# Performance work log

Hardware: AMD Instinct MI355X
Metric: run time of the kernel (lower is better)

The kernel has to match this reference:

```python
import jax, jax.numpy as jnp
import numpy as np

B, L, D = 4, 16384, 128          # batch, voxels per sample, d_model
DI, DS, DTR, K = 256, 16, 8, 4   # d_inner, d_state, dt_rank, conv kernel
N = B * L
EPS = 1e-5


def setup_inputs() -> dict:
    key = jax.random.key(0)
    ks = jax.random.split(key, 12)
    s = 0.02
    feats = jax.random.normal(ks[0], (N, D), jnp.float32)
    coords_xyz = jax.random.randint(ks[1], (N, 3), 0, 1024, jnp.int32)
    # per-batch Morton permutation + its inverse
    perm = jnp.stack([jax.random.permutation(jax.random.fold_in(ks[2], i), L) for i in range(B)]).astype(jnp.int32)
    inv_perm = jnp.argsort(perm, axis=1).astype(jnp.int32)
    return {
        'feats': feats,
        'pos_w': jax.random.normal(ks[3], (3, D), jnp.float32) * s,
        'pos_b': jnp.zeros((D,), jnp.float32),
        'rms_w': jnp.ones((D,), jnp.float32),
        'in_proj_w': jax.random.normal(ks[4], (D, 2 * DI), jnp.float32) * s,
        'conv_w': jax.random.normal(ks[5], (DI, K), jnp.float32) * s,
        'conv_b': jnp.zeros((DI,), jnp.float32),
        'x_proj_w': jax.random.normal(ks[6], (DI, DTR + 2 * DS), jnp.float32) * s,
        'dt_proj_w': jax.random.normal(ks[7], (DTR, DI), jnp.float32) * s,
        'dt_proj_b': jax.random.normal(ks[8], (DI,), jnp.float32) * 0.1,
        'A_log': jnp.log(jnp.broadcast_to(jnp.arange(1.0, DS + 1.0, dtype=jnp.float32), (DI, DS))),
        'D_param': jnp.ones((DI,), jnp.float32),
        'out_proj_w': jax.random.normal(ks[9], (DI, D), jnp.float32) * s,
        'ln_w': jnp.ones((D,), jnp.float32),
        'ln_b': jnp.zeros((D,), jnp.float32),
        'coords_xyz': coords_xyz,
        'perm': perm,
        'inv_perm': inv_perm,
    }


def _gssm(feats, pos_w, pos_b, rms_w, in_proj_w, conv_w, conv_b, x_proj_w,
          dt_proj_w, dt_proj_b, A_log, D_param, out_proj_w, ln_w, ln_b,
          coords_xyz, perm, inv_perm):
    # positional embedding of voxel coords
    pe = coords_xyz.astype(jnp.float32) @ pos_w + pos_b            # [N, D]
    h = (feats + pe).reshape(B, L, D)
    # gather into Morton order (per-batch fancy index)
    hm = jnp.take_along_axis(h, perm[:, :, None].astype(jnp.int32), axis=1)  # [B, L, D]
    # Mamba block: RMSNorm then mixer (block returns mixer output only)
    x = hm * jax.lax.rsqrt(jnp.mean(hm * hm, axis=-1, keepdims=True) + EPS) * rms_w
    xz = x @ in_proj_w                                             # [B, L, 2*DI]
    xi, z = xz[..., :DI], xz[..., DI:]
    # depthwise causal conv1d, kernel K
    xp = jnp.pad(xi, ((0, 0), (K - 1, 0), (0, 0)))
    xc = conv_b + sum(xp[:, j:j + L, :] * conv_w[:, j] for j in range(K))
    xc = jax.nn.silu(xc)                                           # [B, L, DI]
    dbc = xc @ x_proj_w                                            # [B, L, DTR+2*DS]
    dt, Bm, Cm = dbc[..., :DTR], dbc[..., DTR:DTR + DS], dbc[..., DTR + DS:]
    dt = jax.nn.softplus(dt @ dt_proj_w + dt_proj_b)               # [B, L, DI]
    A = -jnp.exp(A_log)                                            # [DI, DS]

    def step(hst, inp):
        x_t, dt_t, b_t, c_t = inp                                  # [B,DI],[B,DI],[B,DS],[B,DS]
        hst = jnp.exp(dt_t[..., None] * A) * hst + (dt_t * x_t)[..., None] * b_t[:, None, :]
        return hst, jnp.einsum('bds,bs->bd', hst, c_t)

    h0 = jnp.zeros((B, DI, DS), xc.dtype)
    _, ys = jax.lax.scan(step, h0, (xc.transpose(1, 0, 2), dt.transpose(1, 0, 2),
                                    Bm.transpose(1, 0, 2), Cm.transpose(1, 0, 2)))
    y = ys.transpose(1, 0, 2) + xc * D_param                       # [B, L, DI]
    y = y * jax.nn.silu(z)
    out = y @ out_proj_w                                           # [B, L, D]
    # scatter back to original voxel order
    out = jnp.take_along_axis(out, inv_perm[:, :, None].astype(jnp.int32), axis=1).reshape(N, D)
    # post-SSM LayerNorm
    mu = jnp.mean(out, axis=-1, keepdims=True)
    var = jnp.mean((out - mu) ** 2, axis=-1, keepdims=True)
    return (out - mu) * jax.lax.rsqrt(var + EPS) * ln_w + ln_b


def reference(feats, pos_w, pos_b, rms_w, in_proj_w, conv_w, conv_b, x_proj_w,
              dt_proj_w, dt_proj_b, A_log, D_param, out_proj_w, ln_w, ln_b,
              coords_xyz, perm, inv_perm):
    return _gssm(feats, pos_w, pos_b, rms_w, in_proj_w, conv_w, conv_b, x_proj_w,
                 dt_proj_w, dt_proj_b, A_log, D_param, out_proj_w, ln_w, ln_b,
                 coords_xyz, perm, inv_perm)
```

## Files before the change

### kernel.cpp

```cpp
#include <hip/hip_runtime.h>
#include <hip/hip_bf16.h>
#include <math.h>

#define B_   4
#define L_   16384
#define D_   128
#define DI_  256
#define DS_  16
#define DTR_ 8
#define N_   65536
#define NC_  128
#define LC_  128
#define TW_  16
#define TP_  260
#define EPS_ 1e-5f

typedef __hip_bfloat16 bf16;
typedef __attribute__((ext_vector_type(8))) short short8;
typedef __attribute__((ext_vector_type(4))) float f32x4;

__device__ __forceinline__ bool probe_bf16(const void* Dp) {
  return ((const unsigned*)Dp)[0] == 0x3F803F80u;
}
__device__ __forceinline__ float ldin(const void* p, size_t i, bool isb) {
  return isb ? __bfloat162float(((const bf16*)p)[i]) : ((const float*)p)[i];
}
__device__ __forceinline__ float4 ld4(const void* p, size_t i4, bool isb) {
  if (!isb) return ((const float4*)p)[i4];
  const ushort4 v = ((const ushort4*)p)[i4];
  float4 r;
  r.x = __uint_as_float((unsigned)v.x << 16);
  r.y = __uint_as_float((unsigned)v.y << 16);
  r.z = __uint_as_float((unsigned)v.z << 16);
  r.w = __uint_as_float((unsigned)v.w << 16);
  return r;
}
__device__ __forceinline__ void splitbf(float v, ushort& hi, ushort& lo) {
  bf16 h = __float2bfloat16(v);
  float rem = v - __bfloat162float(h);
  bf16 l = __float2bfloat16(rem);
  hi = *(ushort*)&h;
  lo = *(ushort*)&l;
}


__global__ __launch_bounds__(256) void k_xnorm(
    const void* __restrict__ feats, const void* __restrict__ pos_w,
    const void* __restrict__ pos_b, const void* __restrict__ rms_w,
    const int* __restrict__ coords, const int* __restrict__ perm,
    const void* __restrict__ Dprobe,
    ushort* __restrict__ xh, ushort* __restrict__ xl) {
  const bool isb = probe_bf16(Dprobe);
  int wv = threadIdx.x >> 6, lane = threadIdx.x & 63;
  int p = blockIdx.x * 4 + wv;
  int b = p >> 14;
  int srow = b * L_ + perm[p];
  float cx = (float)coords[srow*3+0];
  float cy = (float)coords[srow*3+1];
  float cz = (float)coords[srow*3+2];
  int i0 = lane, i1 = lane + 64;
  float h0 = ldin(feats,(size_t)srow*D_ + i0,isb) + cx*ldin(pos_w,i0,isb) + cy*ldin(pos_w,D_+i0,isb)
           + cz*ldin(pos_w,2*D_+i0,isb) + ldin(pos_b,i0,isb);
  float h1 = ldin(feats,(size_t)srow*D_ + i1,isb) + cx*ldin(pos_w,i1,isb) + cy*ldin(pos_w,D_+i1,isb)
           + cz*ldin(pos_w,2*D_+i1,isb) + ldin(pos_b,i1,isb);
  float ss = h0*h0 + h1*h1;
  #pragma unroll
  for (int off = 32; off; off >>= 1) ss += __shfl_xor(ss, off);
  float r = 1.0f / sqrtf(ss * (1.f/128.f) + EPS_);
  float v0 = h0 * r * ldin(rms_w,i0,isb);
  float v1 = h1 * r * ldin(rms_w,i1,isb);
  ushort a, bq;
  splitbf(v0, a, bq);
  xh[(size_t)p*D_ + i0] = a; xl[(size_t)p*D_ + i0] = bq;
  splitbf(v1, a, bq);
  xh[(size_t)p*D_ + i1] = a; xl[(size_t)p*D_ + i1] = bq;
}

__global__ __launch_bounds__(256) void k_prepw(
    const void* __restrict__ Win, const void* __restrict__ Dprobe,
    ushort* __restrict__ wth, ushort* __restrict__ wtl) {
  const bool isb = probe_bf16(Dprobe);
  int idx = blockIdx.x * 256 + threadIdx.x;
  int k = idx >> 9, n = idx & 511;
  float v = ldin(Win, (size_t)k*512 + n, isb);
  ushort a, b;
  splitbf(v, a, b);
  wth[(size_t)n*128 + k] = a;
  wtl[(size_t)n*128 + k] = b;
}

__global__ __launch_bounds__(256) void k_prepxw(
    const void* __restrict__ xW, const void* __restrict__ Dprobe,
    ushort* __restrict__ wxh, ushort* __restrict__ wxl) {
  const bool isb = probe_bf16(Dprobe);
  int idx = blockIdx.x * 256 + threadIdx.x;
  int q = idx >> 8, c = idx & 255;
  float v = (q < 40) ? ldin(xW, (size_t)c*40 + q, isb) : 0.f;
  ushort a, b;
  splitbf(v, a, b);
  wxh[idx] = a;
  wxl[idx] = b;
}

__global__ __launch_bounds__(256) void k_prepdtw(
    const void* __restrict__ dtW, const void* __restrict__ Dprobe,
    ushort* __restrict__ dtwh, ushort* __restrict__ dtwl) {
  const bool isb = probe_bf16(Dprobe);
  int idx = blockIdx.x * 256 + threadIdx.x;
  int d = idx >> 5, k = idx & 31;
  float v = (k < 8) ? ldin(dtW, (size_t)k*256 + d, isb) : 0.f;
  ushort a, b;
  splitbf(v, a, b);
  dtwh[idx] = a;
  dtwl[idx] = b;
}

__global__ __launch_bounds__(256) void k_inproj(
    const ushort* __restrict__ xh, const ushort* __restrict__ xl,
    const ushort* __restrict__ wth, const ushort* __restrict__ wtl,
    float* __restrict__ xiT, float* __restrict__ zB) {
  __shared__ short Ah[64*136];
  __shared__ short Al[64*136];
  __shared__ short Bh[32*136];
  __shared__ short Bl[32*136];
  int tid = threadIdx.x;
  int T0 = blockIdx.x * 64;
  int lane = tid & 63, w = tid >> 6;
  {
    int k0 = (tid & 15) * 8;
    int m0 = tid >> 4;
    #pragma unroll
    for (int mi = 0; mi < 4; ++mi) {
      int m = m0 + 16*mi;
      *(short8*)&Ah[m*136 + k0] = *(const short8*)&xh[(size_t)(T0+m)*128 + k0];
      *(short8*)&Al[m*136 + k0] = *(const short8*)&xl[(size_t)(T0+m)*128 + k0];
    }
  }
  __syncthreads();
  int mloc = lane & 15, quad = lane >> 4;
  short8 afh[4], afl[4];
  #pragma unroll
  for (int ks = 0; ks < 4; ++ks) {
    int ka = ks*32 + quad*8;
    afh[ks] = *(const short8*)&Ah[(w*16 + mloc)*136 + ka];
    afl[ks] = *(const short8*)&Al[(w*16 + mloc)*136 + ka];
  }
  for (int ct = 0; ct < 16; ++ct) {
    int C0 = ct * 32;
    __syncthreads();
    {
      int k0 = (tid & 15) * 8;
      int n0 = tid >> 4;
      #pragma unroll
      for (int ni = 0; ni < 2; ++ni) {
        int n = n0 + 16*ni;
        *(short8*)&Bh[n*136 + k0] = *(const short8*)&wth[(size_t)(C0+n)*128 + k0];
        *(short8*)&Bl[n*136 + k0] = *(const short8*)&wtl[(size_t)(C0+n)*128 + k0];
      }
    }
    __syncthreads();
    #pragma unroll
    for (int nt = 0; nt < 2; ++nt) {
      f32x4 acc = {0.f, 0.f, 0.f, 0.f};
      #pragma unroll
      for (int ks = 0; ks < 4; ++ks) {
        int kb = ks*32 + quad*8;
        short8 bh = *(const short8*)&Bh[(nt*16 + mloc)*136 + kb];
        short8 bl = *(const short8*)&Bl[(nt*16 + mloc)*136 + kb];
        acc = __builtin_amdgcn_mfma_f32_16x16x32_bf16(afh[ks], bh, acc, 0, 0, 0);
        acc = __builtin_amdgcn_mfma_f32_16x16x32_bf16(afl[ks], bh, acc, 0, 0, 0);
        acc = __builtin_amdgcn_mfma_f32_16x16x32_bf16(afh[ks], bl, acc, 0, 0, 0);
      }
      int col = C0 + nt*16 + mloc;
      int trow = T0 + w*16 + quad*4;
      if (col < 256) {
        *(float4*)&xiT[(size_t)col*N_ + trow] = make_float4(acc[0], acc[1], acc[2], acc[3]);
      } else {
        int zc = col - 256;
        #pragma unroll
        for (int r = 0; r < 4; ++r)
          zB[(size_t)(trow + r)*256 + zc] = acc[r];
      }
    }
  }
}

__global__ __launch_bounds__(256) void k_conv_s(
    const float* __restrict__ xiT, const void* __restrict__ conv_w,
    const void* __restrict__ conv_b, const void* __restrict__ Dprobe,
    float* __restrict__ xcT) {
  const bool isb = probe_bf16(Dprobe);
  int idx = blockIdx.x * 256 + threadIdx.x;
  int c = idx >> 16;
  int t = idx & 65535;
  int l = t & (L_-1);
  const float* row = xiT + (size_t)c * N_;
  float acc = ldin(conv_b, c, isb);
  if (l >= 3) acc += row[t-3] * ldin(conv_w, c*4+0, isb);
  if (l >= 2) acc += row[t-2] * ldin(conv_w, c*4+1, isb);
  if (l >= 1) acc += row[t-1] * ldin(conv_w, c*4+2, isb);
  acc += row[t] * ldin(conv_w, c*4+3, isb);
  xcT[(size_t)c*N_ + t] = acc / (1.f + __expf(-acc));
}

__global__ __launch_bounds__(256) void k_xproj(
    const float* __restrict__ xcT,
    const ushort* __restrict__ wxh, const ushort* __restrict__ wxl,
    const ushort* __restrict__ dtwh, const ushort* __restrict__ dtwl,
    const void* __restrict__ dtb, const void* __restrict__ Dprobe,
    float* __restrict__ dtT, float* __restrict__ BmB, float* __restrict__ CmB) {
  const bool isb = probe_bf16(Dprobe);
  __shared__ float s40[64*52];
  __shared__ float sdtb[256];
  const int tid = threadIdx.x;
  const int lane = tid & 63, w = tid >> 6;
  const int T0 = blockIdx.x * 64;
  const int n15 = lane & 15, quad = lane >> 4;
  sdtb[tid] = ldin(dtb, tid, isb);

  f32x4 acc0 = {0.f,0.f,0.f,0.f}, acc1 = {0.f,0.f,0.f,0.f}, acc2 = {0.f,0.f,0.f,0.f};
  const float* xb = &xcT[(size_t)(quad*8)*N_ + T0 + w*16 + n15];
  #pragma unroll
  for (int ks = 0; ks < 8; ++ks) {
    short8 bh, bl;
    #pragma unroll
    for (int j = 0; j < 8; ++j) {
      ushort h, l;
      splitbf(xb[(size_t)(ks*32 + j)*N_], h, l);
      bh[j] = (short)h; bl[j] = (short)l;
    }
    #pragma unroll
    for (int mt = 0; mt < 3; ++mt) {
      const size_t aoff = (size_t)(mt*16 + n15)*256 + ks*32 + quad*8;
      short8 ah = *(const short8*)&wxh[aoff];
      short8 al = *(const short8*)&wxl[aoff];
      f32x4 a = (mt==0) ? acc0 : (mt==1) ? acc1 : acc2;
      a = __builtin_amdgcn_mfma_f32_16x16x32_bf16(ah, bh, a, 0, 0, 0);
      a = __builtin_amdgcn_mfma_f32_16x16x32_bf16(al, bh, a, 0, 0, 0);
      a = __builtin_amdgcn_mfma_f32_16x16x32_bf16(ah, bl, a, 0, 0, 0);
      if (mt==0) acc0 = a; else if (mt==1) acc1 = a; else acc2 = a;
    }
  }
  {
    const int trow = (w*16 + n15)*52;
    #pragma unroll
    for (int r = 0; r < 4; ++r) {
      s40[trow +      quad*4 + r] = acc0[r];
      s40[trow + 16 + quad*4 + r] = acc1[r];
      s40[trow + 32 + quad*4 + r] = acc2[r];
    }
  }
  __syncthreads();
  {
    int t = tid >> 2, fq = tid & 3;
    float4 bm = *(const float4*)&s40[t*52 + 8  + fq*4];
    float4 cm = *(const float4*)&s40[t*52 + 24 + fq*4];
    *(float4*)&BmB[(size_t)(T0+t)*16 + fq*4] = bm;
    *(float4*)&CmB[(size_t)(T0+t)*16 + fq*4] = cm;
  }
  short8 dh, dl;
  #pragma unroll
  for (int j = 0; j < 8; ++j) {
    ushort h, l;
    splitbf(s40[(w*16 + n15)*52 + quad*8 + j], h, l);
    dh[j] = (short)h; dl[j] = (short)l;
  }
  #pragma unroll
  for (int mt = 0; mt < 16; ++mt) {
    f32x4 a = {0.f,0.f,0.f,0.f};
    const size_t doff = (size_t)(mt*16 + n15)*32 + quad*8;
    short8 ah = *(const short8*)&dtwh[doff];
    short8 al = *(const short8*)&dtwl[doff];
    a = __builtin_amdgcn_mfma_f32_16x16x32_bf16(ah, dh, a, 0, 0, 0);
    a = __builtin_amdgcn_mfma_f32_16x16x32_bf16(al, dh, a, 0, 0, 0);
    a = __builtin_amdgcn_mfma_f32_16x16x32_bf16(ah, dl, a, 0, 0, 0);
    #pragma unroll
    for (int r = 0; r < 4; ++r) {
      int d = mt*16 + quad*4 + r;
      float pre = a[r] + sdtb[d];
      float sp = (pre > 20.f) ? pre : log1pf(__expf(pre));
      dtT[(size_t)d*N_ + T0 + w*16 + n15] = sp;
    }
  }
}

__global__ __launch_bounds__(256) void k_scan1(
    const float* __restrict__ dtT, const float* __restrict__ xcT,
    const float* __restrict__ BmB, const void* __restrict__ A_log,
    const void* __restrict__ Dprobe, float* __restrict__ Pb, float* __restrict__ Sb) {
  const bool isb = probe_bf16(Dprobe);
  __shared__ float sdt[TW_*TP_];
  __shared__ float sxc[TW_*TP_];
  __shared__ float sbm[LC_*16];
  int tid = threadIdx.x;
  int blk = blockIdx.x;
  int b = blk >> 7, ch = blk & 127;
  int T0 = b * L_ + ch * LC_;
  int d = tid;
  #pragma unroll
  for (int p = 0; p < 2; ++p) {
    int f = (p*256 + tid) * 4;
    *(float4*)&sbm[f] = *(const float4*)&BmB[(size_t)T0*16 + f];
  }
  float Al[16];
  #pragma unroll
  for (int s = 0; s < 16; ++s) Al[s] = -__expf(ldin(A_log, d*16 + s, isb));
  float h[16];
  #pragma unroll
  for (int s = 0; s < 16; ++s) h[s] = 0.f;
  float sumdt = 0.f;
  for (int it = 0; it < LC_; it += TW_) {
    __syncthreads();
    #pragma unroll
    for (int p = 0; p < 4; ++p) {
      int idx = p*256 + tid;
      int d2 = idx >> 2;
      int i4 = (idx & 3) * 4;
      float4 v = *(const float4*)&dtT[(size_t)d2*N_ + T0 + it + i4];
      float4 w = *(const float4*)&xcT[(size_t)d2*N_ + T0 + it + i4];
      sdt[(i4+0)*TP_ + d2] = v.x; sdt[(i4+1)*TP_ + d2] = v.y;
      sdt[(i4+2)*TP_ + d2] = v.z; sdt[(i4+3)*TP_ + d2] = v.w;
      sxc[(i4+0)*TP_ + d2] = w.x; sxc[(i4+1)*TP_ + d2] = w.y;
      sxc[(i4+2)*TP_ + d2] = w.z; sxc[(i4+3)*TP_ + d2] = w.w;
    }
    __syncthreads();
    #pragma unroll
    for (int i = 0; i < TW_; ++i) {
      float dtv = sdt[i*TP_ + d];
      float xcv = sxc[i*TP_ + d];
      sumdt += dtv;
      float du = dtv * xcv;
      const float* bmr = &sbm[(it+i)*16];
      #pragma unroll
      for (int s = 0; s < 16; ++s)
        h[s] = __expf(dtv * Al[s]) * h[s] + du * bmr[s];
    }
  }
  size_t rec = ((size_t)blk*256 + d) * 16;
  #pragma unroll
  for (int s = 0; s < 16; ++s) {
    Sb[rec + s] = h[s];
    Pb[rec + s] = __expf(Al[s] * sumdt);
  }
}

__global__ __launch_bounds__(256) void k_scan2(
    const float* __restrict__ Pb, const float* __restrict__ Sb, float* __restrict__ Hin) {
  int tid = blockIdx.x * 256 + threadIdx.x;
  int b = tid >> 12, r = tid & 4095;
  float h = 0.f;
  for (int ch = 0; ch < NC_; ++ch) {
    size_t rec = ((size_t)(b*NC_ + ch)) * 4096 + r;
    Hin[rec] = h;
    h = Pb[rec] * h + Sb[rec];
  }
}

__global__ __launch_bounds__(256) void k_scan3(
    const float* __restrict__ dtT, const float* __restrict__ xcT,
    const float* __restrict__ BmB, const float* __restrict__ CmB,
    const void* __restrict__ A_log, const void* __restrict__ Dp,
    const float* __restrict__ Hin, float* __restrict__ zyg) {
  const bool isb = probe_bf16(Dp);
  __shared__ float sdt[TW_*TP_];
  __shared__ float sxc[TW_*TP_];
  __shared__ float sbm[LC_*16];
  __shared__ float scm[LC_*16];
  int tid = threadIdx.x;
  int blk = blockIdx.x;
  int b = blk >> 7, ch = blk & 127;
  int T0 = b * L_ + ch * LC_;
  int d = tid;
  #pragma unroll
  for (int p = 0; p < 2; ++p) {
    int f = (p*256 + tid) * 4;
    *(float4*)&sbm[f] = *(const float4*)&BmB[(size_t)T0*16 + f];
    *(float4*)&scm[f] = *(const float4*)&CmB[(size_t)T0*16 + f];
  }
  float Al[16];
  #pragma unroll
  for (int s = 0; s < 16; ++s) Al[s] = -__expf(ldin(A_log, d*16 + s, isb));
  float h[16];
  size_t rec = ((size_t)blk*256 + d) * 16;
  #pragma unroll
  for (int s = 0; s < 16; ++s) h[s] = Hin[rec + s];
  float Dv = ldin(Dp, d, isb);
  for (int it = 0; it < LC_; it += TW_) {
    __syncthreads();
    #pragma unroll
    for (int p = 0; p < 4; ++p) {
      int idx = p*256 + tid;
      int d2 = idx >> 2;
      int i4 = (idx & 3) * 4;
      float4 v = *(const float4*)&dtT[(size_t)d2*N_ + T0 + it + i4];
      float4 w = *(const float4*)&xcT[(size_t)d2*N_ + T0 + it + i4];
      sdt[(i4+0)*TP_ + d2] = v.x; sdt[(i4+1)*TP_ + d2] = v.y;
      sdt[(i4+2)*TP_ + d2] = v.z; sdt[(i4+3)*TP_ + d2] = v.w;
      sxc[(i4+0)*TP_ + d2] = w.x; sxc[(i4+1)*TP_ + d2] = w.y;
      sxc[(i4+2)*TP_ + d2] = w.z; sxc[(i4+3)*TP_ + d2] = w.w;
    }
    __syncthreads();
    #pragma unroll
    for (int i = 0; i < TW_; ++i) {
      float dtv = sdt[i*TP_ + d];
      float xcv = sxc[i*TP_ + d];
      float du = dtv * xcv;
      const float* bmr = &sbm[(it+i)*16];
      const float* cmr = &scm[(it+i)*16];
      float y = 0.f;
      #pragma unroll
      for (int s = 0; s < 16; ++s) {
        h[s] = __expf(dtv * Al[s]) * h[s] + du * bmr[s];
        y += h[s] * cmr[s];
      }
      float yv = y + xcv * Dv;
      size_t zi = (size_t)(T0 + it + i)*256 + d;
      float zv = zyg[zi];
      float sil = zv / (1.f + __expf(-zv));
      zyg[zi] = yv * sil;
    }
  }
}

__global__ __launch_bounds__(256) void k_outproj(
    const float* __restrict__ yg, const void* __restrict__ W2,
    const void* __restrict__ Dprobe, float* __restrict__ outp) {
  const bool isb = probe_bf16(Dprobe);
  __shared__ float As[64*68];
  __shared__ float Bs[64*128];
  int tid = threadIdx.x;
  int T0 = blockIdx.x * 64;
  int tm = tid & 15, tn = tid >> 4;
  float acc[4][8] = {{0.f}};
  for (int kb = 0; kb < 256; kb += 64) {
    {
      int m = tid & 63, kq = tid >> 6;
      #pragma unroll
      for (int r = 0; r < 4; ++r) {
        int k0 = kq*16 + r*4;
        float4 v = *(const float4*)&yg[(size_t)(T0+m)*256 + kb + k0];
        As[(k0+0)*68+m] = v.x; As[(k0+1)*68+m] = v.y;
        As[(k0+2)*68+m] = v.z; As[(k0+3)*68+m] = v.w;
      }
      int n = (tid & 31)*4, kq2 = tid >> 5;
      #pragma unroll
      for (int p = 0; p < 8; ++p) {
        int k = kq2 + p*8;
        float4 w = ld4(W2, ((size_t)(kb+k)*128 + n) >> 2, isb);
        *(float4*)&Bs[k*128 + n] = w;
      }
    }
    __syncthreads();
    #pragma unroll 4
    for (int k = 0; k < 64; ++k) {
      float4 a  = *(const float4*)&As[k*68 + tm*4];
      float4 b0 = *(const float4*)&Bs[k*128 + tn*8];
      float4 b1 = *(const float4*)&Bs[k*128 + tn*8 + 4];
      float am[4] = {a.x, a.y, a.z, a.w};
      float bn[8] = {b0.x, b0.y, b0.z, b0.w, b1.x, b1.y, b1.z, b1.w};
      #pragma unroll
      for (int mi = 0; mi < 4; ++mi)
        #pragma unroll
        for (int ni = 0; ni < 8; ++ni)
          acc[mi][ni] += am[mi] * bn[ni];
    }
    __syncthreads();
  }
  #pragma unroll
  for (int mi = 0; mi < 4; ++mi) {
    size_t m = (size_t)(T0 + tm*4 + mi);
    *(float4*)&outp[m*128 + tn*8]     = make_float4(acc[mi][0], acc[mi][1], acc[mi][2], acc[mi][3]);
    *(float4*)&outp[m*128 + tn*8 + 4] = make_float4(acc[mi][4], acc[mi][5], acc[mi][6], acc[mi][7]);
  }
}

__global__ __launch_bounds__(256) void k_ln(
    const float* __restrict__ outp, const int* __restrict__ perm,
    const void* __restrict__ ln_w, const void* __restrict__ ln_b,
    const void* __restrict__ Dprobe, void* __restrict__ out) {
  const bool isb = probe_bf16(Dprobe);
  int wv = threadIdx.x >> 6, lane = threadIdx.x & 63;
  int p = blockIdx.x * 4 + wv;
  int b = p >> 14;
  int dest = b * L_ + perm[p];
  float v0 = outp[(size_t)p*128 + lane];
  float v1 = outp[(size_t)p*128 + lane + 64];
  float s1 = v0 + v1, s2 = v0*v0 + v1*v1;
  #pragma unroll
  for (int off = 32; off; off >>= 1) {
    s1 += __shfl_xor(s1, off);
    s2 += __shfl_xor(s2, off);
  }
  float mean = s1 * (1.f/128.f);
  float var  = s2 * (1.f/128.f) - mean*mean;
  float r = 1.0f / sqrtf(var + EPS_);
  float o0 = (v0 - mean)*r*ldin(ln_w,lane,isb)    + ldin(ln_b,lane,isb);
  float o1 = (v1 - mean)*r*ldin(ln_w,lane+64,isb) + ldin(ln_b,lane+64,isb);
  if (isb) {
    ((bf16*)out)[(size_t)dest*128 + lane]      = __float2bfloat16(o0);
    ((bf16*)out)[(size_t)dest*128 + lane + 64] = __float2bfloat16(o1);
  } else {
    ((float*)out)[(size_t)dest*128 + lane]      = o0;
    ((float*)out)[(size_t)dest*128 + lane + 64] = o1;
  }
}

extern "C" void kernel_launch(void* const* d_in, const int* in_sizes, int n_in,
                              void* d_out, int out_size, void* d_ws, size_t ws_size,
                              hipStream_t stream) {
  const void* feats    = d_in[0];
  const void* pos_w    = d_in[1];
  const void* pos_b    = d_in[2];
  const void* rms_w    = d_in[3];
  const void* in_proj  = d_in[4];
  const void* conv_w   = d_in[5];
  const void* conv_b   = d_in[6];
  const void* x_proj   = d_in[7];
  const void* dt_projw = d_in[8];
  const void* dt_projb = d_in[9];
  const void* A_log    = d_in[10];
  const void* D_param  = d_in[11];
  const void* out_proj = d_in[12];
  const void* ln_w     = d_in[13];
  const void* ln_b     = d_in[14];
  const int*  coords   = (const int*)d_in[15];
  const int*  perm     = (const int*)d_in[16];

  float* ws = (float*)d_ws;
  const size_t NN = (size_t)N_;
  ushort* xh  = (ushort*)ws;
  ushort* xl  = (ushort*)(ws + 64*NN);
  ushort* wth = (ushort*)(ws + 640*NN);
  ushort* wtl = (ushort*)(ws + 641*NN);
  ushort* wxh  = (ushort*)ws;
  ushort* wxl  = ((ushort*)ws) + 12288;
  ushort* dtwh = ((ushort*)ws) + 24576;
  ushort* dtwl = ((ushort*)ws) + 32768;
  float* Pb   = ws;
  float* Sb   = ws + 32*NN;
  float* Hin  = ws + 64*NN;
  float* BmB  = ws + 96*NN;
  float* CmB  = ws + 112*NN;
  float* xiT  = ws + 128*NN;
  float* dtT  = ws + 128*NN;
  float* outp = ws + 128*NN;
  float* zB   = ws + 384*NN;
  float* yg   = zB;
  float* xcT  = ws + 640*NN;

  k_prepw<<<256, 256, 0, stream>>>(in_proj, D_param, wth, wtl);
  k_xnorm<<<N_/4, 256, 0, stream>>>(feats, pos_w, pos_b, rms_w, coords, perm, D_param, xh, xl);
  k_inproj<<<N_/64, 256, 0, stream>>>(xh, xl, wth, wtl, xiT, zB);
  k_prepxw<<<48, 256, 0, stream>>>(x_proj, D_param, wxh, wxl);
  k_prepdtw<<<32, 256, 0, stream>>>(dt_projw, D_param, dtwh, dtwl);
  k_conv_s<<<(DI_*N_)/256, 256, 0, stream>>>(xiT, conv_w, conv_b, D_param, xcT);
  k_xproj<<<N_/64, 256, 0, stream>>>(xcT, wxh, wxl, dtwh, dtwl, dt_projb, D_param, dtT, BmB, CmB);
  k_scan1<<<B_*NC_, 256, 0, stream>>>(dtT, xcT, BmB, A_log, D_param, Pb, Sb);
  k_scan2<<<64, 256, 0, stream>>>(Pb, Sb, Hin);
  k_scan3<<<B_*NC_, 256, 0, stream>>>(dtT, xcT, BmB, CmB, A_log, D_param, Hin, zB);
  k_outproj<<<N_/64, 256, 0, stream>>>(yg, out_proj, D_param, outp);
  k_ln<<<N_/4, 256, 0, stream>>>(outp, perm, ln_w, ln_b, D_param, d_out);
}
```

Measured before the change: 557.7 us.

## Exploit A=-(s+1) structure in scan, transpose z layout, shorten scan chunks

The scan kernels now check at runtime whether A rows are integer multiples of A[0], and if so compute the per-state decay as successive powers of one exponential instead of 16 exps. Each thread reads its own channel's dt/x/z rows directly with float4 loads instead of staging a transposed tile through shared memory, and z/y are stored channel-major so scan3 and outproj load contiguously. Chunk length is halved to 64 with twice as many chunks, raising parallelism but lengthening scan2's serial carry loop. The power trick depends on the A_log initialisation pattern, with a fallback path for other values, and repeated multiplication may accumulate slightly more rounding error.

```diff
diff --git a/kernel.cpp b/kernel.cpp
--- a/kernel.cpp
+++ b/kernel.cpp
@@ -9,10 +9,10 @@
 #define DS_  16
 #define DTR_ 8
 #define N_   65536
-#define NC_  128
-#define LC_  128
+#define NC_  256
+#define NCS_ 8
+#define LC_  64
 #define TW_  16
-#define TP_  260
 #define EPS_ 1e-5f
 
 typedef __hip_bfloat16 bf16;
@@ -118,7 +118,7 @@
 __global__ __launch_bounds__(256) void k_inproj(
     const ushort* __restrict__ xh, const ushort* __restrict__ xl,
     const ushort* __restrict__ wth, const ushort* __restrict__ wtl,
-    float* __restrict__ xiT, float* __restrict__ zB) {
+    float* __restrict__ xiT, float* __restrict__ zT) {
   __shared__ short Ah[64*136];
   __shared__ short Al[64*136];
   __shared__ short Bh[32*136];
@@ -176,10 +176,7 @@
       if (col < 256) {
         *(float4*)&xiT[(size_t)col*N_ + trow] = make_float4(acc[0], acc[1], acc[2], acc[3]);
       } else {
-        int zc = col - 256;
-        #pragma unroll
-        for (int r = 0; r < 4; ++r)
-          zB[(size_t)(trow + r)*256 + zc] = acc[r];
+        *(float4*)&zT[(size_t)(col-256)*N_ + trow] = make_float4(acc[0], acc[1], acc[2], acc[3]);
       }
     }
   }
@@ -278,62 +275,89 @@
     for (int r = 0; r < 4; ++r) {
       int d = mt*16 + quad*4 + r;
       float pre = a[r] + sdtb[d];
-      float sp = (pre > 20.f) ? pre : log1pf(__expf(pre));
+      float sp = (pre > 20.f) ? pre : __logf(1.f + __expf(pre));
       dtT[(size_t)d*N_ + T0 + w*16 + n15] = sp;
     }
   }
 }
 
-__global__ __launch_bounds__(256) void k_scan1(
+__global__ __launch_bounds__(256, 4) void k_scan1(
     const float* __restrict__ dtT, const float* __restrict__ xcT,
     const float* __restrict__ BmB, const void* __restrict__ A_log,
     const void* __restrict__ Dprobe, float* __restrict__ Pb, float* __restrict__ Sb) {
   const bool isb = probe_bf16(Dprobe);
-  __shared__ float sdt[TW_*TP_];
-  __shared__ float sxc[TW_*TP_];
   __shared__ float sbm[LC_*16];
-  int tid = threadIdx.x;
-  int blk = blockIdx.x;
-  int b = blk >> 7, ch = blk & 127;
-  int T0 = b * L_ + ch * LC_;
-  int d = tid;
-  #pragma unroll
-  for (int p = 0; p < 2; ++p) {
-    int f = (p*256 + tid) * 4;
+  const int tid = threadIdx.x;
+  const int blk = blockIdx.x;
+  const int b = blk >> NCS_, ch = blk & (NC_-1);
+  const int T0 = b * L_ + ch * LC_;
+  const int d = tid;
+  {
+    int f = tid * 4;
     *(float4*)&sbm[f] = *(const float4*)&BmB[(size_t)T0*16 + f];
   }
   float Al[16];
   #pragma unroll
   for (int s = 0; s < 16; ++s) Al[s] = -__expf(ldin(A_log, d*16 + s, isb));
+  bool fast = true;
+  #pragma unroll
+  for (int s = 1; s < 16; ++s)
+    fast = fast && (fabsf(Al[s] - (float)(s+1) * Al[0]) <= 1e-4f * fabsf(Al[s]));
+  __syncthreads();
   float h[16];
   #pragma unroll
   for (int s = 0; s < 16; ++s) h[s] = 0.f;
   float sumdt = 0.f;
+  const float* dp = dtT + (size_t)d*N_ + T0;
+  const float* xp = xcT + (size_t)d*N_ + T0;
   for (int it = 0; it < LC_; it += TW_) {
-    __syncthreads();
-    #pragma unroll
-    for (int p = 0; p < 4; ++p) {
-      int idx = p*256 + tid;
-      int d2 = idx >> 2;
-      int i4 = (idx & 3) * 4;
-      float4 v = *(const float4*)&dtT[(size_t)d2*N_ + T0 + it + i4];
-      float4 w = *(const float4*)&xcT[(size_t)d2*N_ + T0 + it + i4];
-      sdt[(i4+0)*TP_ + d2] = v.x; sdt[(i4+1)*TP_ + d2] = v.y;
-      sdt[(i4+2)*TP_ + d2] = v.z; sdt[(i4+3)*TP_ + d2] = v.w;
-      sxc[(i4+0)*TP_ + d2] = w.x; sxc[(i4+1)*TP_ + d2] = w.y;
-      sxc[(i4+2)*TP_ + d2] = w.z; sxc[(i4+3)*TP_ + d2] = w.w;
-    }
-    __syncthreads();
-    #pragma unroll
-    for (int i = 0; i < TW_; ++i) {
-      float dtv = sdt[i*TP_ + d];
-      float xcv = sxc[i*TP_ + d];
-      sumdt += dtv;
-      float du = dtv * xcv;
-      const float* bmr = &sbm[(it+i)*16];
+    float4 fd[4], fx[4];
+    #pragma unroll
+    for (int j = 0; j < 4; ++j) {
+      fd[j] = *(const float4*)&dp[it + j*4];
+      fx[j] = *(const float4*)&xp[it + j*4];
+    }
+    #pragma unroll
+    for (int j = 0; j < 4; ++j) {
+      float dts[4] = {fd[j].x, fd[j].y, fd[j].z, fd[j].w};
+      float xcs[4] = {fx[j].x, fx[j].y, fx[j].z, fx[j].w};
       #pragma unroll
-      for (int s = 0; s < 16; ++s)
-        h[s] = __expf(dtv * Al[s]) * h[s] + du * bmr[s];
+      for (int k = 0; k < 4; ++k) {
+        float dtv = dts[k];
+        float xcv = xcs[k];
+        sumdt += dtv;
+        float du = dtv * xcv;
+        const int row = (it + j*4 + k)*16;
+        const float4 b0 = *(const float4*)&sbm[row];
+        const float4 b1 = *(const float4*)&sbm[row + 4];
+        const float4 b2 = *(const float4*)&sbm[row + 8];
+        const float4 b3 = *(const float4*)&sbm[row + 12];
+        if (fast) {
+          float e1 = __expf(dtv * Al[0]);
+          float p = e1;
+          h[0]  = p*h[0]  + du*b0.x; p *= e1;
+          h[1]  = p*h[1]  + du*b0.y; p *= e1;
+          h[2]  = p*h[2]  + du*b0.z; p *= e1;
+          h[3]  = p*h[3]  + du*b0.w; p *= e1;
+          h[4]  = p*h[4]  + du*b1.x; p *= e1;
+          h[5]  = p*h[5]  + du*b1.y; p *= e1;
+          h[6]  = p*h[6]  + du*b1.z; p *= e1;
+          h[7]  = p*h[7]  + du*b1.w; p *= e1;
+          h[8]  = p*h[8]  + du*b2.x; p *= e1;
+          h[9]  = p*h[9]  + du*b2.y; p *= e1;
+          h[10] = p*h[10] + du*b2.z; p *= e1;
+          h[11] = p*h[11] + du*b2.w; p *= e1;
+          h[12] = p*h[12] + du*b3.x; p *= e1;
+          h[13] = p*h[13] + du*b3.y; p *= e1;
+          h[14] = p*h[14] + du*b3.z; p *= e1;
+          h[15] = p*h[15] + du*b3.w;
+        } else {
+          const float* bmr = &sbm[row];
+          #pragma unroll
+          for (int s = 0; s < 16; ++s)
+            h[s] = __expf(dtv * Al[s]) * h[s] + du * bmr[s];
+        }
+      }
     }
   }
   size_t rec = ((size_t)blk*256 + d) * 16;
@@ -356,68 +380,103 @@
   }
 }
 
-__global__ __launch_bounds__(256) void k_scan3(
+__global__ __launch_bounds__(256, 4) void k_scan3(
     const float* __restrict__ dtT, const float* __restrict__ xcT,
     const float* __restrict__ BmB, const float* __restrict__ CmB,
     const void* __restrict__ A_log, const void* __restrict__ Dp,
-    const float* __restrict__ Hin, float* __restrict__ zyg) {
+    const float* __restrict__ Hin, float* __restrict__ zyT) {
   const bool isb = probe_bf16(Dp);
-  __shared__ float sdt[TW_*TP_];
-  __shared__ float sxc[TW_*TP_];
   __shared__ float sbm[LC_*16];
   __shared__ float scm[LC_*16];
-  int tid = threadIdx.x;
-  int blk = blockIdx.x;
-  int b = blk >> 7, ch = blk & 127;
-  int T0 = b * L_ + ch * LC_;
-  int d = tid;
-  #pragma unroll
-  for (int p = 0; p < 2; ++p) {
-    int f = (p*256 + tid) * 4;
+  const int tid = threadIdx.x;
+  const int blk = blockIdx.x;
+  const int b = blk >> NCS_, ch = blk & (NC_-1);
+  const int T0 = b * L_ + ch * LC_;
+  const int d = tid;
+  {
+    int f = tid * 4;
     *(float4*)&sbm[f] = *(const float4*)&BmB[(size_t)T0*16 + f];
     *(float4*)&scm[f] = *(const float4*)&CmB[(size_t)T0*16 + f];
   }
   float Al[16];
   #pragma unroll
   for (int s = 0; s < 16; ++s) Al[s] = -__expf(ldin(A_log, d*16 + s, isb));
+  bool fast = true;
+  #pragma unroll
+  for (int s = 1; s < 16; ++s)
+    fast = fast && (fabsf(Al[s] - (float)(s+1) * Al[0]) <= 1e-4f * fabsf(Al[s]));
   float h[16];
   size_t rec = ((size_t)blk*256 + d) * 16;
   #pragma unroll
   for (int s = 0; s < 16; ++s) h[s] = Hin[rec + s];
-  float Dv = ldin(Dp, d, isb);
+  const float Dv = ldin(Dp, d, isb);
+  __syncthreads();
+  const float* dp = dtT + (size_t)d*N_ + T0;
+  const float* xp = xcT + (size_t)d*N_ + T0;
+  float* zp = zyT + (size_t)d*N_ + T0;
   for (int it = 0; it < LC_; it += TW_) {
-    __syncthreads();
-    #pragma unroll
-    for (int p = 0; p < 4; ++p) {
-      int idx = p*256 + tid;
-      int d2 = idx >> 2;
-      int i4 = (idx & 3) * 4;
-      float4 v = *(const float4*)&dtT[(size_t)d2*N_ + T0 + it + i4];
-      float4 w = *(const float4*)&xcT[(size_t)d2*N_ + T0 + it + i4];
-      sdt[(i4+0)*TP_ + d2] = v.x; sdt[(i4+1)*TP_ + d2] = v.y;
-      sdt[(i4+2)*TP_ + d2] = v.z; sdt[(i4+3)*TP_ + d2] = v.w;
-      sxc[(i4+0)*TP_ + d2] = w.x; sxc[(i4+1)*TP_ + d2] = w.y;
-      sxc[(i4+2)*TP_ + d2] = w.z; sxc[(i4+3)*TP_ + d2] = w.w;
-    }
-    __syncthreads();
-    #pragma unroll
-    for (int i = 0; i < TW_; ++i) {
-      float dtv = sdt[i*TP_ + d];
-      float xcv = sxc[i*TP_ + d];
-      float du = dtv * xcv;
-      const float* bmr = &sbm[(it+i)*16];
-      const float* cmr = &scm[(it+i)*16];
-      float y = 0.f;
+    float4 fd[4], fx[4], fz[4];
+    #pragma unroll
+    for (int j = 0; j < 4; ++j) {
+      fd[j] = *(const float4*)&dp[it + j*4];
+      fx[j] = *(const float4*)&xp[it + j*4];
+      fz[j] = *(const float4*)&zp[it + j*4];
+    }
+    #pragma unroll
+    for (int j = 0; j < 4; ++j) {
+      float dts[4] = {fd[j].x, fd[j].y, fd[j].z, fd[j].w};
+      float xcs[4] = {fx[j].x, fx[j].y, fx[j].z, fx[j].w};
+      float zs[4]  = {fz[j].x, fz[j].y, fz[j].z, fz[j].w};
+      float ov[4];
       #pragma unroll
-      for (int s = 0; s < 16; ++s) {
-        h[s] = __expf(dtv * Al[s]) * h[s] + du * bmr[s];
-        y += h[s] * cmr[s];
+      for (int k = 0; k < 4; ++k) {
+        float dtv = dts[k];
+        float xcv = xcs[k];
+        float du = dtv * xcv;
+        const int row = (it + j*4 + k)*16;
+        const float4 b0 = *(const float4*)&sbm[row];
+        const float4 b1 = *(const float4*)&sbm[row + 4];
+        const float4 b2 = *(const float4*)&sbm[row + 8];
+        const float4 b3 = *(const float4*)&sbm[row + 12];
+        const float4 c0 = *(const float4*)&scm[row];
+        const float4 c1 = *(const float4*)&scm[row + 4];
+        const float4 c2 = *(const float4*)&scm[row + 8];
+        const float4 c3 = *(const float4*)&scm[row + 12];
+        float yp = 0.f;
+        if (fast) {
+          float e1 = __expf(dtv * Al[0]);
+          float p = e1;
+          h[0]  = p*h[0]  + du*b0.x; yp += h[0] *c0.x; p *= e1;
+          h[1]  = p*h[1]  + du*b0.y; yp += h[1] *c0.y; p *= e1;
+          h[2]  = p*h[2]  + du*b0.z; yp += h[2] *c0.z; p *= e1;
+          h[3]  = p*h[3]  + du*b0.w; yp += h[3] *c0.w; p *= e1;
+          h[4]  = p*h[4]  + du*b1.x; yp += h[4] *c1.x; p *= e1;
+          h[5]  = p*h[5]  + du*b1.y; yp += h[5] *c1.y; p *= e1;
+          h[6]  = p*h[6]  + du*b1.z; yp += h[6] *c1.z; p *= e1;
+          h[7]  = p*h[7]  + du*b1.w; yp += h[7] *c1.w; p *= e1;
+          h[8]  = p*h[8]  + du*b2.x; yp += h[8] *c2.x; p *= e1;
+          h[9]  = p*h[9]  + du*b2.y; yp += h[9] *c2.y; p *= e1;
+          h[10] = p*h[10] + du*b2.z; yp += h[10]*c2.z; p *= e1;
+          h[11] = p*h[11] + du*b2.w; yp += h[11]*c2.w; p *= e1;
+          h[12] = p*h[12] + du*b3.x; yp += h[12]*c3.x; p *= e1;
+          h[13] = p*h[13] + du*b3.y; yp += h[13]*c3.y; p *= e1;
+          h[14] = p*h[14] + du*b3.z; yp += h[14]*c3.z; p *= e1;
+          h[15] = p*h[15] + du*b3.w; yp += h[15]*c3.w;
+        } else {
+          const float* bmr = &sbm[row];
+          const float* cmr = &scm[row];
+          #pragma unroll
+          for (int s = 0; s < 16; ++s) {
+            h[s] = __expf(dtv * Al[s]) * h[s] + du * bmr[s];
+            yp += h[s] * cmr[s];
+          }
+        }
+        float yv = yp + xcv * Dv;
+        float zvv = zs[k];
+        float sil = zvv / (1.f + __expf(-zvv));
+        ov[k] = yv * sil;
       }
-      float yv = y + xcv * Dv;
-      size_t zi = (size_t)(T0 + it + i)*256 + d;
-      float zv = zyg[zi];
-      float sil = zv / (1.f + __expf(-zv));
-      zyg[zi] = yv * sil;
+      *(float4*)&zp[it + j*4] = make_float4(ov[0], ov[1], ov[2], ov[3]);
     }
   }
 }
@@ -434,20 +493,19 @@
   float acc[4][8] = {{0.f}};
   for (int kb = 0; kb < 256; kb += 64) {
     {
-      int m = tid & 63, kq = tid >> 6;
+      int k = tid >> 2, mq = (tid & 3) * 16;
+      const float* src = &yg[(size_t)(kb + k)*N_ + T0 + mq];
       #pragma unroll
       for (int r = 0; r < 4; ++r) {
-        int k0 = kq*16 + r*4;
-        float4 v = *(const float4*)&yg[(size_t)(T0+m)*256 + kb + k0];
-        As[(k0+0)*68+m] = v.x; As[(k0+1)*68+m] = v.y;
-        As[(k0+2)*68+m] = v.z; As[(k0+3)*68+m] = v.w;
+        float4 v = *(const float4*)&src[r*4];
+        *(float4*)&As[k*68 + mq + r*4] = v;
       }
       int n = (tid & 31)*4, kq2 = tid >> 5;
       #pragma unroll
       for (int p = 0; p < 8; ++p) {
-        int k = kq2 + p*8;
-        float4 w = ld4(W2, ((size_t)(kb+k)*128 + n) >> 2, isb);
-        *(float4*)&Bs[k*128 + n] = w;
+        int k2 = kq2 + p*8;
+        float4 w = ld4(W2, ((size_t)(kb+k2)*128 + n) >> 2, isb);
+        *(float4*)&Bs[k2*128 + n] = w;
       }
     }
     __syncthreads();
@@ -536,28 +594,28 @@
   ushort* wxl  = ((ushort*)ws) + 12288;
   ushort* dtwh = ((ushort*)ws) + 24576;
   ushort* dtwl = ((ushort*)ws) + 32768;
-  float* Pb   = ws;
-  float* Sb   = ws + 32*NN;
-  float* Hin  = ws + 64*NN;
   float* BmB  = ws + 96*NN;
   float* CmB  = ws + 112*NN;
   float* xiT  = ws + 128*NN;
   float* dtT  = ws + 128*NN;
   float* outp = ws + 128*NN;
-  float* zB   = ws + 384*NN;
-  float* yg   = zB;
+  float* Pb   = ws + 192*NN;
+  float* Sb   = ws + 256*NN;
+  float* Hin  = ws + 320*NN;
+  float* zT   = ws + 384*NN;
+  float* yg   = zT;
   float* xcT  = ws + 640*NN;
 
   k_prepw<<<256, 256, 0, stream>>>(in_proj, D_param, wth, wtl);
   k_xnorm<<<N_/4, 256, 0, stream>>>(feats, pos_w, pos_b, rms_w, coords, perm, D_param, xh, xl);
-  k_inproj<<<N_/64, 256, 0, stream>>>(xh, xl, wth, wtl, xiT, zB);
+  k_inproj<<<N_/64, 256, 0, stream>>>(xh, xl, wth, wtl, xiT, zT);
   k_prepxw<<<48, 256, 0, stream>>>(x_proj, D_param, wxh, wxl);
   k_prepdtw<<<32, 256, 0, stream>>>(dt_projw, D_param, dtwh, dtwl);
   k_conv_s<<<(DI_*N_)/256, 256, 0, stream>>>(xiT, conv_w, conv_b, D_param, xcT);
   k_xproj<<<N_/64, 256, 0, stream>>>(xcT, wxh, wxl, dtwh, dtwl, dt_projb, D_param, dtT, BmB, CmB);
   k_scan1<<<B_*NC_, 256, 0, stream>>>(dtT, xcT, BmB, A_log, D_param, Pb, Sb);
   k_scan2<<<64, 256, 0, stream>>>(Pb, Sb, Hin);
-  k_scan3<<<B_*NC_, 256, 0, stream>>>(dtT, xcT, BmB, CmB, A_log, D_param, Hin, zB);
+  k_scan3<<<B_*NC_, 256, 0, stream>>>(dtT, xcT, BmB, CmB, A_log, D_param, Hin, zT);
   k_outproj<<<N_/64, 256, 0, stream>>>(yg, out_proj, D_param, outp);
   k_ln<<<N_/4, 256, 0, stream>>>(outp, perm, ln_w, ln_b, D_param, d_out);
 }
```

Result: faster. 537.7 us (-3.6%).
